# Kernel tuning notes

Hardware: AMD Instinct MI355X
Metric: run time of the kernel (lower is better)

The kernel has to match this reference:

```python
import jax, jax.numpy as jnp
import numpy as np
from jax import lax

C, H, W_ = 256, 384, 384

def setup_inputs() -> dict:
    key = jax.random.key(0)
    k1, k2, k3, k4 = jax.random.split(key, 4)
    return {
        'input1': jax.random.normal(k1, (1, C, H, W_), dtype=jnp.float32),
        'input2': jax.random.normal(k2, (1, C, H, W_), dtype=jnp.float32),
        'W': jax.random.normal(k3, (C, C, 3, 3), dtype=jnp.float32) * (1.0 / np.sqrt(C * 9)),
        'b': jax.random.normal(k4, (C,), dtype=jnp.float32) * 0.01,
    }

def _conv(x, W, b):
    # nn.Conv2d(C, C, 3, stride=1, padding=0)
    y = lax.conv_general_dilated(x, W, window_strides=(1, 1), padding='VALID',
                                 dimension_numbers=('NCHW', 'OIHW', 'NCHW'))
    return y + b[None, :, None, None]

def _ca(x):
    # adaptive_avg_pool2d to (1,1) then sigmoid -> [1, C, 1, 1]
    return jax.nn.sigmoid(jnp.mean(x, axis=(2, 3), keepdims=True))

def reference(input1, input2, W, b):
    input3 = input1 + input2
    x1 = _ca(_conv(input1, W, b))
    x2 = _ca(_conv(input2, W, b))
    x3 = _ca(_conv(input3, W, b))
    # Vectorized replication of the per-channel branch logic (ties: x1==x2 fires both blocks)
    c1 = x1 >= x2
    c2 = x1 <= x2
    dt = input1.dtype
    adj1 = (c1 & (x1 >= x3)).astype(dt)
    adj2 = (c2 & (x2 >= x3)).astype(dt)
    adj3 = ((c1 & (x1 < x3)) | (c2 & (x2 < x3))).astype(dt)
    return adj1 * input1 + adj2 * input2 + adj3 * input3
```

## Files before the change

kernel.cpp:

```cpp
#include <hip/hip_runtime.h>


#define CH 256
#define WD 384
#define ROW_F4 96
#define CH_F4 (WD * WD / 4)
#define CH_ELEMS (WD * WD)
#define NCHUNK 4
#define CHUNK_ROWS 96
#define CHUNK_F4 (CHUNK_ROWS * ROW_F4)

typedef float v4f __attribute__((ext_vector_type(4)));

__device__ inline double wave_reduce(double v) {
    #pragma unroll
    for (int off = 32; off > 0; off >>= 1)
        v += __shfl_down(v, off, 64);
    return v;
}

__global__ __launch_bounds__(256, 8) void sumsA_kernel(
    const float* __restrict__ in1, const float* __restrict__ in2,
    double* __restrict__ P )
{
    int bid   = blockIdx.x;
    int chunk = bid & 3;
    int c     = (bid >> 2) & 255;
    int inp   = bid >> 10;
    const float4* p = (const float4*)((inp ? in2 : in1) + (size_t)c * CH_ELEMS)
                      + (size_t)chunk * CHUNK_F4;
    int tid = threadIdx.x;

    double T0 = 0, T1 = 0, T2 = 0, T3 = 0;
    #pragma unroll 3
    for (int k = 0; k < 36; k += 4) {
        float4 v0 = p[tid + (k + 0) * 256];
        float4 v1 = p[tid + (k + 1) * 256];
        float4 v2 = p[tid + (k + 2) * 256];
        float4 v3 = p[tid + (k + 3) * 256];
        T0 += ((double)v0.x + (double)v0.y) + ((double)v0.z + (double)v0.w);
        T1 += ((double)v1.x + (double)v1.y) + ((double)v1.z + (double)v1.w);
        T2 += ((double)v2.x + (double)v2.y) + ((double)v2.z + (double)v2.w);
        T3 += ((double)v3.x + (double)v3.y) + ((double)v3.z + (double)v3.w);
    }
    double T = (T0 + T1) + (T2 + T3);

    double C0 = 0, C1 = 0, C382 = 0, C383 = 0;
    if (tid < CHUNK_ROWS) {
        float4 a = p[tid * ROW_F4];
        float4 z = p[tid * ROW_F4 + ROW_F4 - 1];
        C0 = a.x; C1 = a.y; C382 = z.z; C383 = z.w;
    }
    double R0 = 0, R1 = 0, R382 = 0, R383 = 0;
    if (chunk == 0 && tid < 2 * ROW_F4) {
        float4 v = p[tid];
        double s = ((double)v.x + (double)v.y) + ((double)v.z + (double)v.w);
        if (tid < ROW_F4) R0 = s; else R1 = s;
    }
    if (chunk == 3 && tid < 2 * ROW_F4) {
        float4 v = p[CHUNK_F4 - 2 * ROW_F4 + tid];
        double s = ((double)v.x + (double)v.y) + ((double)v.z + (double)v.w);
        if (tid < ROW_F4) R382 = s; else R383 = s;
    }

    __shared__ double red[4][9];
    double vals[9] = {T, C0, C1, C382, C383, R0, R1, R382, R383};
    int lane = tid & 63, wv = tid >> 6;
    #pragma unroll
    for (int k = 0; k < 9; k++) {
        double r = wave_reduce(vals[k]);
        if (lane == 0) red[wv][k] = r;
    }
    __syncthreads();
    if (tid < 9) {
        P[(size_t)bid * 9 + tid] =
            (red[0][tid] + red[1][tid]) + (red[2][tid] + red[3][tid]);
    }
}

__global__ __launch_bounds__(64) void sumsB_kernel(
    const float* __restrict__ in1, const float* __restrict__ in2,
    const double* __restrict__ P, double* __restrict__ S )
{
    int b = blockIdx.x;
    int inp = b >> 8, c = b & 255;
    int tid = threadIdx.x;
    __shared__ double a[9];
    if (tid < 9) {
        const double* pp = P + (size_t)b * 36 + tid;
        a[tid] = (pp[0] + pp[9]) + (pp[18] + pp[27]);
    }
    __syncthreads();
    if (tid == 0) {
        const float* base = (inp ? in2 : in1) + (size_t)c * CH_ELEMS;
        double Tt = a[0], c0 = a[1], c1 = a[2], c382 = a[3], c383 = a[4];
        double r0 = a[5], r1 = a[6], r382 = a[7], r383 = a[8];

        double x00 = base[0*WD+0],   x01 = base[0*WD+1],   x0a = base[0*WD+382],   x0b = base[0*WD+383];
        double x10 = base[1*WD+0],   x11 = base[1*WD+1],   x1a = base[1*WD+382],   x1b = base[1*WD+383];
        double xa0 = base[382*WD+0], xa1 = base[382*WD+1], xaa = base[382*WD+382], xab = base[382*WD+383];
        double xb0 = base[383*WD+0], xb1 = base[383*WD+1], xba = base[383*WD+382], xbb = base[383*WD+383];

        double Tot[3] = { Tt - c382 - c383, Tt - c0 - c383, Tt - c0 - c1 };
        double rp0[3] = { r0 - x0a - x0b,   r0 - x00 - x0b,   r0 - x00 - x01 };
        double rp1[3] = { r1 - x1a - x1b,   r1 - x10 - x1b,   r1 - x10 - x11 };
        double rpa[3] = { r382 - xaa - xab, r382 - xa0 - xab, r382 - xa0 - xa1 };
        double rpb[3] = { r383 - xba - xbb, r383 - xb0 - xbb, r383 - xb0 - xb1 };

        double* out = S + (size_t)b * 9;
        #pragma unroll
        for (int kw = 0; kw < 3; kw++) {
            out[0*3 + kw] = Tot[kw] - rpa[kw] - rpb[kw];
            out[1*3 + kw] = Tot[kw] - rp0[kw] - rpb[kw];
            out[2*3 + kw] = Tot[kw] - rp0[kw] - rp1[kw];
        }
    }
}

__global__ __launch_bounds__(256) void coef_kernel(
    const float* __restrict__ Wt, const float* __restrict__ b,
    const double* __restrict__ S, float* __restrict__ K )
{
    int co = blockIdx.x;
    int tid = threadIdx.x;
    const float*  wrow = Wt + (size_t)co * 2304;
    const double* S1 = S;
    const double* S2 = S + 2304;
    double y1 = 0, y2 = 0;
    for (int j = tid; j < 2304; j += 256) {
        double w = (double)wrow[j];
        y1 += w * S1[j];
        y2 += w * S2[j];
    }
    __shared__ double red[4][2];
    int lane = tid & 63, wv = tid >> 6;
    y1 = wave_reduce(y1);
    y2 = wave_reduce(y2);
    if (lane == 0) { red[wv][0] = y1; red[wv][1] = y2; }
    __syncthreads();
    if (tid == 0) {
        double Y1 = (red[0][0] + red[1][0]) + (red[2][0] + red[3][0]);
        double Y2 = (red[0][1] + red[1][1]) + (red[2][1] + red[3][1]);
        const double inv = 1.0 / 145924.0;
        double bb = (double)b[co];
        double m1 = bb + Y1 * inv;
        double m2 = bb + Y2 * inv;
        double m3 = bb + (Y1 + Y2) * inv;
        bool c1 = (m1 >= m2), c2 = (m1 <= m2);
        float adj1 = (c1 && m1 >= m3) ? 1.0f : 0.0f;
        float adj2 = (c2 && m2 >= m3) ? 1.0f : 0.0f;
        float adj3 = ((c1 && m1 < m3) || (c2 && m2 < m3)) ? 1.0f : 0.0f;
        K[2*co]     = adj1 + adj3;
        K[2*co + 1] = adj2 + adj3;
    }
}

__global__ __launch_bounds__(256) void mix_kernel(
    const float* __restrict__ in1, const float* __restrict__ in2,
    const float* __restrict__ K, float* __restrict__ out)
{
    int c = blockIdx.y;
    size_t idx = (size_t)c * CH_F4 + (size_t)blockIdx.x * 512 + threadIdx.x;
    const float4* a4 = (const float4*)in1;
    const float4* b4 = (const float4*)in2;
    v4f* o4 = (v4f*)out;
    float k1 = K[2*c], k2 = K[2*c + 1];
    float4 a0 = a4[idx],       b0 = b4[idx];
    float4 a1 = a4[idx + 256], b1 = b4[idx + 256];
    v4f o0, o1;
    o0.x = k1*a0.x + k2*b0.x; o0.y = k1*a0.y + k2*b0.y;
    o0.z = k1*a0.z + k2*b0.z; o0.w = k1*a0.w + k2*b0.w;
    o1.x = k1*a1.x + k2*b1.x; o1.y = k1*a1.y + k2*b1.y;
    o1.z = k1*a1.z + k2*b1.z; o1.w = k1*a1.w + k2*b1.w;
    __builtin_nontemporal_store(o0, &o4[idx]);
    __builtin_nontemporal_store(o1, &o4[idx + 256]);
}

extern "C" void kernel_launch(void* const* d_in, const int* in_sizes, int n_in,
                              void* d_out, int out_size, void* d_ws, size_t ws_size,
                              hipStream_t stream) {
    const float* in1 = (const float*)d_in[0];
    const float* in2 = (const float*)d_in[1];
    const float* Wt  = (const float*)d_in[2];
    const float* b   = (const float*)d_in[3];
    float* out = (float*)d_out;

    double* P = (double*)d_ws;
    double* S = (double*)((char*)d_ws + 2 * CH * NCHUNK * 9 * sizeof(double));
    float*  K = (float*)((char*)S + 2 * CH * 9 * sizeof(double));

    sumsA_kernel<<<2 * CH * NCHUNK, 256, 0, stream>>>(in1, in2, P);
    sumsB_kernel<<<2 * CH, 64, 0, stream>>>(in1, in2, P, S);
    coef_kernel<<<CH, 256, 0, stream>>>(Wt, b, S, K);
    mix_kernel<<<dim3(CH_F4 / 512, CH), 256, 0, stream>>>(in1, in2, K, out);
}
```

Measured before the change: 413.2 us.

## Merge the two-stage sum kernels into one and skip unused input loads in mix

```diff
diff --git a/kernel.cpp b/kernel.cpp
--- a/kernel.cpp
+++ b/kernel.cpp
@@ -6,9 +6,6 @@
 #define ROW_F4 96
 #define CH_F4 (WD * WD / 4)
 #define CH_ELEMS (WD * WD)
-#define NCHUNK 4
-#define CHUNK_ROWS 96
-#define CHUNK_F4 (CHUNK_ROWS * ROW_F4)
 
 typedef float v4f __attribute__((ext_vector_type(4)));
 
@@ -19,21 +16,18 @@
     return v;
 }
 
-__global__ __launch_bounds__(256, 8) void sumsA_kernel(
+__global__ __launch_bounds__(256) void sums_kernel(
     const float* __restrict__ in1, const float* __restrict__ in2,
-    double* __restrict__ P )
+    double* __restrict__ S )
 {
-    int bid   = blockIdx.x;
-    int chunk = bid & 3;
-    int c     = (bid >> 2) & 255;
-    int inp   = bid >> 10;
-    const float4* p = (const float4*)((inp ? in2 : in1) + (size_t)c * CH_ELEMS)
-                      + (size_t)chunk * CHUNK_F4;
+    int b   = blockIdx.x;
+    int inp = b >> 8, c = b & 255;
+    const float4* p = (const float4*)((inp ? in2 : in1) + (size_t)c * CH_ELEMS);
     int tid = threadIdx.x;
 
     double T0 = 0, T1 = 0, T2 = 0, T3 = 0;
-    #pragma unroll 3
-    for (int k = 0; k < 36; k += 4) {
+    #pragma unroll 4
+    for (int k = 0; k < 144; k += 4) {
         float4 v0 = p[tid + (k + 0) * 256];
         float4 v1 = p[tid + (k + 1) * 256];
         float4 v2 = p[tid + (k + 2) * 256];
@@ -45,22 +39,24 @@
     }
     double T = (T0 + T1) + (T2 + T3);
 
+    __shared__ float4 cornA[4], cornZ[4];
     double C0 = 0, C1 = 0, C382 = 0, C383 = 0;
-    if (tid < CHUNK_ROWS) {
-        float4 a = p[tid * ROW_F4];
-        float4 z = p[tid * ROW_F4 + ROW_F4 - 1];
-        C0 = a.x; C1 = a.y; C382 = z.z; C383 = z.w;
+    for (int r = tid; r < 384; r += 256) {
+        float4 a = p[r * ROW_F4];
+        float4 z = p[r * ROW_F4 + ROW_F4 - 1];
+        C0 += a.x; C1 += a.y; C382 += z.z; C383 += z.w;
+        if (r < 2)    { cornA[r]       = a; cornZ[r]       = z; }
+        if (r >= 382) { cornA[r - 380] = a; cornZ[r - 380] = z; }
     }
+
     double R0 = 0, R1 = 0, R382 = 0, R383 = 0;
-    if (chunk == 0 && tid < 2 * ROW_F4) {
+    if (tid < 2 * ROW_F4) {
         float4 v = p[tid];
         double s = ((double)v.x + (double)v.y) + ((double)v.z + (double)v.w);
         if (tid < ROW_F4) R0 = s; else R1 = s;
-    }
-    if (chunk == 3 && tid < 2 * ROW_F4) {
-        float4 v = p[CHUNK_F4 - 2 * ROW_F4 + tid];
-        double s = ((double)v.x + (double)v.y) + ((double)v.z + (double)v.w);
-        if (tid < ROW_F4) R382 = s; else R383 = s;
+        float4 w = p[382 * ROW_F4 + tid];
+        double t = ((double)w.x + (double)w.y) + ((double)w.z + (double)w.w);
+        if (tid < ROW_F4) R382 = t; else R383 = t;
     }
 
     __shared__ double red[4][9];
@@ -72,34 +68,22 @@
         if (lane == 0) red[wv][k] = r;
     }
     __syncthreads();
-    if (tid < 9) {
-        P[(size_t)bid * 9 + tid] =
-            (red[0][tid] + red[1][tid]) + (red[2][tid] + red[3][tid]);
-    }
-}
 
-__global__ __launch_bounds__(64) void sumsB_kernel(
-    const float* __restrict__ in1, const float* __restrict__ in2,
-    const double* __restrict__ P, double* __restrict__ S )
-{
-    int b = blockIdx.x;
-    int inp = b >> 8, c = b & 255;
-    int tid = threadIdx.x;
-    __shared__ double a[9];
-    if (tid < 9) {
-        const double* pp = P + (size_t)b * 36 + tid;
-        a[tid] = (pp[0] + pp[9]) + (pp[18] + pp[27]);
-    }
-    __syncthreads();
     if (tid == 0) {
-        const float* base = (inp ? in2 : in1) + (size_t)c * CH_ELEMS;
-        double Tt = a[0], c0 = a[1], c1 = a[2], c382 = a[3], c383 = a[4];
-        double r0 = a[5], r1 = a[6], r382 = a[7], r383 = a[8];
+        double Tt   = (red[0][0] + red[1][0]) + (red[2][0] + red[3][0]);
+        double c0   = (red[0][1] + red[1][1]) + (red[2][1] + red[3][1]);
+        double c1   = (red[0][2] + red[1][2]) + (red[2][2] + red[3][2]);
+        double c382 = (red[0][3] + red[1][3]) + (red[2][3] + red[3][3]);
+        double c383 = (red[0][4] + red[1][4]) + (red[2][4] + red[3][4]);
+        double r0   = (red[0][5] + red[1][5]) + (red[2][5] + red[3][5]);
+        double r1   = (red[0][6] + red[1][6]) + (red[2][6] + red[3][6]);
+        double r382 = (red[0][7] + red[1][7]) + (red[2][7] + red[3][7]);
+        double r383 = (red[0][8] + red[1][8]) + (red[2][8] + red[3][8]);
 
-        double x00 = base[0*WD+0],   x01 = base[0*WD+1],   x0a = base[0*WD+382],   x0b = base[0*WD+383];
-        double x10 = base[1*WD+0],   x11 = base[1*WD+1],   x1a = base[1*WD+382],   x1b = base[1*WD+383];
-        double xa0 = base[382*WD+0], xa1 = base[382*WD+1], xaa = base[382*WD+382], xab = base[382*WD+383];
-        double xb0 = base[383*WD+0], xb1 = base[383*WD+1], xba = base[383*WD+382], xbb = base[383*WD+383];
+        double x00 = cornA[0].x, x01 = cornA[0].y, x0a = cornZ[0].z, x0b = cornZ[0].w;
+        double x10 = cornA[1].x, x11 = cornA[1].y, x1a = cornZ[1].z, x1b = cornZ[1].w;
+        double xa0 = cornA[2].x, xa1 = cornA[2].y, xaa = cornZ[2].z, xab = cornZ[2].w;
+        double xb0 = cornA[3].x, xb1 = cornA[3].y, xba = cornZ[3].z, xbb = cornZ[3].w;
 
         double Tot[3] = { Tt - c382 - c383, Tt - c0 - c383, Tt - c0 - c1 };
         double rp0[3] = { r0 - x0a - x0b,   r0 - x00 - x0b,   r0 - x00 - x01 };
@@ -165,13 +149,23 @@
     const float4* b4 = (const float4*)in2;
     v4f* o4 = (v4f*)out;
     float k1 = K[2*c], k2 = K[2*c + 1];
-    float4 a0 = a4[idx],       b0 = b4[idx];
-    float4 a1 = a4[idx + 256], b1 = b4[idx + 256];
     v4f o0, o1;
-    o0.x = k1*a0.x + k2*b0.x; o0.y = k1*a0.y + k2*b0.y;
-    o0.z = k1*a0.z + k2*b0.z; o0.w = k1*a0.w + k2*b0.w;
-    o1.x = k1*a1.x + k2*b1.x; o1.y = k1*a1.y + k2*b1.y;
-    o1.z = k1*a1.z + k2*b1.z; o1.w = k1*a1.w + k2*b1.w;
+    if (k2 == 0.0f) {
+        float4 a0 = a4[idx], a1 = a4[idx + 256];
+        o0.x = k1*a0.x; o0.y = k1*a0.y; o0.z = k1*a0.z; o0.w = k1*a0.w;
+        o1.x = k1*a1.x; o1.y = k1*a1.y; o1.z = k1*a1.z; o1.w = k1*a1.w;
+    } else if (k1 == 0.0f) {
+        float4 b0 = b4[idx], b1 = b4[idx + 256];
+        o0.x = k2*b0.x; o0.y = k2*b0.y; o0.z = k2*b0.z; o0.w = k2*b0.w;
+        o1.x = k2*b1.x; o1.y = k2*b1.y; o1.z = k2*b1.z; o1.w = k2*b1.w;
+    } else {
+        float4 a0 = a4[idx],       b0 = b4[idx];
+        float4 a1 = a4[idx + 256], b1 = b4[idx + 256];
+        o0.x = k1*a0.x + k2*b0.x; o0.y = k1*a0.y + k2*b0.y;
+        o0.z = k1*a0.z + k2*b0.z; o0.w = k1*a0.w + k2*b0.w;
+        o1.x = k1*a1.x + k2*b1.x; o1.y = k1*a1.y + k2*b1.y;
+        o1.z = k1*a1.z + k2*b1.z; o1.w = k1*a1.w + k2*b1.w;
+    }
     __builtin_nontemporal_store(o0, &o4[idx]);
     __builtin_nontemporal_store(o1, &o4[idx + 256]);
 }
@@ -185,12 +179,10 @@
     const float* b   = (const float*)d_in[3];
     float* out = (float*)d_out;
 
-    double* P = (double*)d_ws;
-    double* S = (double*)((char*)d_ws + 2 * CH * NCHUNK * 9 * sizeof(double));
-    float*  K = (float*)((char*)S + 2 * CH * 9 * sizeof(double));
+    double* S = (double*)d_ws;
+    float*  K = (float*)((char*)d_ws + 2 * CH * 9 * sizeof(double));
 
-    sumsA_kernel<<<2 * CH * NCHUNK, 256, 0, stream>>>(in1, in2, P);
-    sumsB_kernel<<<2 * CH, 64, 0, stream>>>(in1, in2, P, S);
+    sums_kernel<<<2 * CH, 256, 0, stream>>>(in1, in2, S);
     coef_kernel<<<CH, 256, 0, stream>>>(Wt, b, S, K);
     mix_kernel<<<dim3(CH_F4 / 512, CH), 256, 0, stream>>>(in1, in2, K, out);
 }
```

Measured after the change: 397.0 us. 3.9% less time.
